# Performance work log

Hardware: AMD Instinct MI355X
Metric: run time of the kernel (lower is better)

The kernel has to match this reference:

```python
import jax, jax.numpy as jnp
import numpy as np

HEADS = 20


def cape_embed(f, P):
    # f: [b, s, d], P: [b, s, 4, 4]; rotate channel groups of 4 by P
    b, s, d = f.shape
    f4 = f.reshape(b, s, d // 4, 4)
    out = jnp.einsum('bsik,bskj->bsij', f4, P)
    return out.reshape(b, s, d)


def setup_inputs() -> dict:
    key = jax.random.key(0)
    ks = jax.random.split(key, 9)
    bt, l, d = 2, 1024, 1280  # (b*t_out, tokens, channels)
    t_out, b = 2, 1
    sd = 1.0 / np.sqrt(d)
    return {
        'hidden_states': jax.random.normal(ks[0], (bt, l, d), jnp.float32),
        'p_out': jax.random.normal(ks[1], (b, t_out, 4, 4), jnp.float32) * 0.5,
        'p_out_inv': jax.random.normal(ks[2], (b, t_out, 4, 4), jnp.float32) * 0.5,
        'Wq': jax.random.normal(ks[3], (d, d), jnp.float32) * sd,
        'Wk': jax.random.normal(ks[4], (d, d), jnp.float32) * sd,
        'Wv': jax.random.normal(ks[5], (d, d), jnp.float32) * sd,
        'Wo': jax.random.normal(ks[6], (d, d), jnp.float32) * sd,
        'bo': jnp.zeros((d,), jnp.float32),
    }


def reference(hidden_states, p_out, p_out_inv, Wq, Wk, Wv, Wo, bo):
    residual = hidden_states  # [(b t_out), l, d]
    b = p_out.shape[0]
    t_out = p_out.shape[1]
    bt, l, d = hidden_states.shape
    s = t_out * l
    hd = d // HEADS
    scale = hd ** -0.5

    # rearrange '(b t_out) l d -> b (t_out l) d'
    hs = hidden_states.reshape(b, s, d)

    q = hs @ Wq
    k = hs @ Wk
    v = hs @ Wv

    # repeat per-frame CAPE matrices over spatial tokens: 'b t f g -> b (t l) f g'
    Pq = jnp.repeat(p_out_inv, l, axis=1)  # [b, s, 4, 4]
    Pk = jnp.repeat(p_out, l, axis=1)      # self-attn: p_in := p_out
    q = cape_embed(q, Pq)
    k = cape_embed(k, Pk)

    # head split: [b, s, d] -> [b, h, s, hd]
    qh = q.reshape(b, s, HEADS, hd).transpose(0, 2, 1, 3)
    kh = k.reshape(b, s, HEADS, hd).transpose(0, 2, 1, 3)
    vh = v.reshape(b, s, HEADS, hd).transpose(0, 2, 1, 3)

    scores = jnp.einsum('bhsd,bhtd->bhst', qh, kh) * scale
    probs = jax.nn.softmax(scores, axis=-1)
    out = jnp.einsum('bhst,bhtd->bhsd', probs, vh)

    out = out.transpose(0, 2, 1, 3).reshape(b, s, d)
    out = out @ Wo + bo

    # rearrange 'b (t_out l) d -> (b t_out) l d'
    out = out.reshape(bt, l, d)
    out = out + residual  # residual_connection; rescale_output_factor = 1.0
    return out
```

## Files before the change

### kernel.cpp

```cpp
#include <hip/hip_runtime.h>

typedef short short8 __attribute__((ext_vector_type(8)));
typedef short short4v __attribute__((ext_vector_type(4)));
typedef float f32x4 __attribute__((ext_vector_type(4)));
typedef float float4v __attribute__((ext_vector_type(4)));
typedef __bf16 bf16x8 __attribute__((ext_vector_type(8)));
typedef _Float16 half4 __attribute__((ext_vector_type(4)));
typedef _Float16 half2v __attribute__((ext_vector_type(2)));

__device__ __forceinline__ short f2bf(float x) {
  unsigned u = __builtin_bit_cast(unsigned, x);
  u += 0x7fffu + ((u >> 16) & 1u);
  return (short)(u >> 16);
}

__device__ __forceinline__ f32x4 mfma16(short8 a, short8 b, f32x4 c) {
  return __builtin_amdgcn_mfma_f32_16x16x32_bf16(
      __builtin_bit_cast(bf16x8, a), __builtin_bit_cast(bf16x8, b), c, 0, 0, 0);
}

__device__ __forceinline__ void async16(void* lds, const void* g) {
  __builtin_amdgcn_global_load_lds(
      (const __attribute__((address_space(1))) unsigned*)g,
      (__attribute__((address_space(3))) unsigned*)lds, 16, 0, 0);
}

__global__ __launch_bounds__(256) void capeT_all_kernel(
    const float* __restrict__ Wq, const float* __restrict__ Wk,
    const float* __restrict__ Wv, const float* __restrict__ Wo,
    const float* __restrict__ p_inv, const float* __restrict__ p_out,
    float qscale, short* __restrict__ BT0, short* __restrict__ BT1,
    short* __restrict__ wo_t, const float* __restrict__ hs,
    short* __restrict__ hs_bf) {
  const int ND = 1280, KD = 1280;
  const size_t SEC = (size_t)1280 * 1280;
  int z = blockIdx.z;
  int tx = threadIdx.x, ty = threadIdx.y;
  if (z == 4) {
    int t = ty * 32 + tx;
    int base = ((blockIdx.y * 40 + blockIdx.x) * 256 + t) * 2;
    const int n4 = 2048 * 1280 / 4;
#pragma unroll
    for (int r = 0; r < 2; r++) {
      int i = base + r;
      if (i < n4) {
        float4v v = *(const float4v*)(hs + (size_t)i * 4);
        short4v o;
#pragma unroll
        for (int j = 0; j < 4; j++) o[j] = f2bf(v[j]);
        *(short4v*)(hs_bf + (size_t)i * 4) = o;
      }
    }
    return;
  }
  const float* W;
  const float* P;
  float scale = 1.0f;
  short *d0, *d1;
  if (z == 0) { W = Wq; P = p_inv; scale = qscale; d0 = BT0; d1 = BT1; }
  else if (z == 1) { W = Wk; P = p_out; d0 = BT0 + SEC; d1 = BT1 + SEC; }
  else if (z == 2) { W = Wv; P = nullptr; d0 = BT0 + 2 * SEC; d1 = BT1 + 2 * SEC; }
  else { W = Wo; P = nullptr; d0 = wo_t; d1 = nullptr; }

  __shared__ float tile[32][33];
  int bn = blockIdx.x * 32, bk = blockIdx.y * 32;
  for (int i = ty; i < 32; i += 8)
    tile[i][tx] = W[(size_t)(bk + i) * ND + bn + tx];
  __syncthreads();
  for (int c = ty; c < 32; c += 8) {
    float v0, v1;
    if (P) {
      int g = c & ~3, jj = c & 3;
      float a0 = 0.f, a1 = 0.f;
#pragma unroll
      for (int j = 0; j < 4; j++) {
        float wv = tile[tx][g + j];
        a0 += wv * P[j * 4 + jj];
        a1 += wv * P[16 + j * 4 + jj];
      }
      v0 = a0 * scale;
      v1 = a1 * scale;
    } else {
      v0 = v1 = tile[tx][c] * scale;
    }
    size_t o = (size_t)(bn + c) * KD + bk + tx;
    d0[o] = f2bf(v0);
    if (d1) d1[o] = f2bf(v1);
  }
}


__global__ __launch_bounds__(256) void gemm128_qkv_kernel(
    const short* __restrict__ A, const short* __restrict__ B0,
    const short* __restrict__ B1, int M, int N, int K,
    short* __restrict__ qb, short* __restrict__ ktl,
    _Float16* __restrict__ vtl) {
  __shared__ __align__(16) short As[2][128][32];
  __shared__ __align__(16) short Bs[2][128][32];
  int tid = threadIdx.x;
  int l = tid & 63, w = tid >> 6;
  int wr = w >> 1, wc = w & 1;
  int lr = l & 15, lg = l >> 4;
  int bm = blockIdx.y * 128, bn = blockIdx.x * 128;
  const short* BT = (bm >= 1024) ? B1 : B0;
  f32x4 acc[4][4] = {};

  auto stage = [&](int b, int k0) {
    const short* ga = A + (size_t)(bm + (tid >> 2)) * K + k0 + (tid & 3) * 8;
    const short* gb = BT + (size_t)(bn + (tid >> 2)) * K + k0 + (tid & 3) * 8;
    char* la = (char*)&As[b][0][0] + w * 1024;
    char* lb = (char*)&Bs[b][0][0] + w * 1024;
    async16(la, ga);
    async16(la + 4096, ga + (size_t)64 * K);
    async16(lb, gb);
    async16(lb + 4096, gb + (size_t)64 * K);
  };

  auto compute = [&](int b) {
    const short* Ab = &As[b][0][0];
    const short* Bb = &Bs[b][0][0];
    short8 af[4], bf_[4];
#pragma unroll
    for (int mi = 0; mi < 4; mi++)
      af[mi] = *(const short8*)(Ab + (wr * 64 + mi * 16 + lr) * 32 + lg * 8);
#pragma unroll
    for (int nj = 0; nj < 4; nj++)
      bf_[nj] = *(const short8*)(Bb + (wc * 64 + nj * 16 + lr) * 32 + lg * 8);
#pragma unroll
    for (int mi = 0; mi < 4; mi++)
#pragma unroll
      for (int nj = 0; nj < 4; nj++)
        acc[mi][nj] = mfma16(af[mi], bf_[nj], acc[mi][nj]);
  };

  int nk = K >> 5;
  stage(0, 0);
  for (int ks = 0; ks < nk; ks += 2) {
    __syncthreads();
    if (ks + 1 < nk) stage(1, (ks + 1) << 5);
    compute(0);
    __syncthreads();
    if (ks + 2 < nk) stage(0, (ks + 2) << 5);
    compute(1);
  }

#pragma unroll
  for (int mi = 0; mi < 4; mi++)
#pragma unroll
    for (int nj = 0; nj < 4; nj++)
#pragma unroll
      for (int i = 0; i < 4; i++) {
        int row = bm + wr * 64 + mi * 16 + lg * 4 + i;
        int col = bn + wc * 64 + nj * 16 + lr;
        float v = acc[mi][nj][i];
        int s = row;
        if (col < 1280) {
          qb[(((size_t)(col >> 6)) * 2048 + s) * 64 + (col & 63)] = f2bf(v);
        } else if (col < 2560) {
          int cc = col - 1280;
          int h = cc >> 6, d = cc & 63;
          int kt = s >> 6, r = s & 63;
          int kcol = (((d >> 3) ^ (r & 7)) << 3) | (d & 7);
          ktl[(((size_t)h * 32 + kt) * 64 + r) * 64 + kcol] = f2bf(v);
        } else {
          int cc = col - 2560;
          int h = cc >> 6, dv = cc & 63;
          int kt = s >> 6, key = s & 63;
          int sub = key >> 5, k5 = key & 31;
          int g = k5 >> 2;
          int vidx = sub * 2048 + g * 256 + ((dv ^ g) << 2) + (k5 & 3);
          vtl[((size_t)h * 32 + kt) * 4096 + vidx] = (_Float16)v;
        }
      }
}


__global__ __launch_bounds__(256) void gemm64_o_kernel(
    const short* __restrict__ A, const short* __restrict__ BT,
    int M, int N, int K, const float* __restrict__ bias,
    const float* __restrict__ resid, float* __restrict__ out) {
  __shared__ __align__(16) short As[2][64][32];
  __shared__ __align__(16) short Bs[2][64][32];
  int tid = threadIdx.x;
  int l = tid & 63, w = tid >> 6;
  int wr = w >> 1, wc = w & 1;
  int lr = l & 15, lg = l >> 4;
  int bm = blockIdx.y * 64, bn = blockIdx.x * 64;
  f32x4 acc[2][2] = {};

  auto stage = [&](int b, int k0) {
    const short* ga = A + (size_t)(bm + (tid >> 2)) * K + k0 + (tid & 3) * 8;
    const short* gb = BT + (size_t)(bn + (tid >> 2)) * K + k0 + (tid & 3) * 8;
    async16((char*)&As[b][0][0] + w * 1024, ga);
    async16((char*)&Bs[b][0][0] + w * 1024, gb);
  };

  auto compute = [&](int b) {
    const short* Ab = &As[b][0][0];
    const short* Bb = &Bs[b][0][0];
    short8 af[2], bf_[2];
#pragma unroll
    for (int mi = 0; mi < 2; mi++)
      af[mi] = *(const short8*)(Ab + (wr * 32 + mi * 16 + lr) * 32 + lg * 8);
#pragma unroll
    for (int nj = 0; nj < 2; nj++)
      bf_[nj] = *(const short8*)(Bb + (wc * 32 + nj * 16 + lr) * 32 + lg * 8);
#pragma unroll
    for (int mi = 0; mi < 2; mi++)
#pragma unroll
      for (int nj = 0; nj < 2; nj++)
        acc[mi][nj] = mfma16(af[mi], bf_[nj], acc[mi][nj]);
  };

  int nk = K >> 5;
  stage(0, 0);
  for (int ks = 0; ks < nk; ks += 2) {
    __syncthreads();
    if (ks + 1 < nk) stage(1, (ks + 1) << 5);
    compute(0);
    __syncthreads();
    if (ks + 2 < nk) stage(0, (ks + 2) << 5);
    compute(1);
  }

#pragma unroll
  for (int mi = 0; mi < 2; mi++)
#pragma unroll
    for (int nj = 0; nj < 2; nj++)
#pragma unroll
      for (int i = 0; i < 4; i++) {
        int row = bm + wr * 32 + mi * 16 + lg * 4 + i;
        int col = bn + wc * 32 + nj * 16 + lr;
        out[(size_t)row * N + col] =
            acc[mi][nj][i] + bias[col] + resid[(size_t)row * N + col];
      }
}

__global__ __launch_bounds__(256) void attn_kernel(
    const short* __restrict__ qb, const short* __restrict__ k_tiled,
    const _Float16* __restrict__ v_tiled, float* __restrict__ opart,
    float2* __restrict__ ml) {
  const int S = 2048, HD = 64;
  int h = blockIdx.x;
  int qblk = blockIdx.y;
  int half = blockIdx.z;
  int sbase = half * 32;
  int tid = threadIdx.x;
  int w = tid >> 6, l = tid & 63;
  int lr = l & 15, lg = l >> 4;
  int q0 = qblk * 64 + w * 16;

  __shared__ __align__(16) short Kl[2][32][64];
  __shared__ __align__(16) _Float16 Vl[2][2048];

  const short* qptr = qb + ((size_t)h * S + q0 + lr) * HD;
  short8 qf0 = *(const short8*)(qptr + lg * 8);
  short8 qf1 = *(const short8*)(qptr + 32 + lg * 8);

  auto stageKV = [&](int b, int ts) {
    int kt = ts >> 1, sub = ts & 1;
    const short* gk = k_tiled + ((size_t)h * 32 + kt) * 4096 + sub * 2048 + tid * 8;
    const _Float16* gv = v_tiled + ((size_t)h * 32 + kt) * 4096 + sub * 2048 + tid * 8;
    async16((char*)&Kl[b][0][0] + w * 1024, gk);
    async16((char*)&Vl[b][0] + w * 1024, gv);
  };

  float m = -1e30f, lsum = 0.f;
  f32x4 oacc[4] = {};

  auto compute_tile = [&](int buf) {
    const short* Kb = &Kl[buf][0][0];
    const _Float16* Vb = &Vl[buf][0];
    f32x4 st[2];
    __builtin_amdgcn_s_setprio(1);
#pragma unroll
    for (int kk = 0; kk < 2; kk++) {
      int r = kk * 16 + lr;
      int sw = r & 7;
      short8 kf0 = *(const short8*)(Kb + r * 64 + ((lg ^ sw) << 3));
      short8 kf1 = *(const short8*)(Kb + r * 64 + (((4 + lg) ^ sw) << 3));
      f32x4 s0 = {};
      s0 = mfma16(kf0, qf0, s0);
      s0 = mfma16(kf1, qf1, s0);
      st[kk] = s0;
    }
    __builtin_amdgcn_s_setprio(0);
    float m0 = fmaxf(fmaxf(st[0][0], st[0][1]), fmaxf(st[0][2], st[0][3]));
    float m1 = fmaxf(fmaxf(st[1][0], st[1][1]), fmaxf(st[1][2], st[1][3]));
    float pmax = fmaxf(m0, m1);
    if (!__all(pmax <= m + 8.0f)) {
      float tm = pmax;
      tm = fmaxf(tm, __shfl_xor(tm, 16));
      tm = fmaxf(tm, __shfl_xor(tm, 32));
      float mnew = fmaxf(m, tm);
      float fac = __builtin_amdgcn_exp2f(m - mnew);
      lsum *= fac;
#pragma unroll
      for (int i = 0; i < 4; i++) {
        float fi = __shfl(fac, lg * 4 + i);
#pragma unroll
        for (int nb = 0; nb < 4; nb++) oacc[nb][i] *= fi;
      }
      m = mnew;
    }
    half4 pf[2];
    float ps[2];
#pragma unroll
    for (int kk = 0; kk < 2; kk++) {
      float p0 = __builtin_amdgcn_exp2f(st[kk][0] - m);
      float p1 = __builtin_amdgcn_exp2f(st[kk][1] - m);
      float p2 = __builtin_amdgcn_exp2f(st[kk][2] - m);
      float p3 = __builtin_amdgcn_exp2f(st[kk][3] - m);
      half2v lo = __builtin_bit_cast(half2v, __builtin_amdgcn_cvt_pkrtz(p0, p1));
      half2v hi = __builtin_bit_cast(half2v, __builtin_amdgcn_cvt_pkrtz(p2, p3));
      pf[kk][0] = lo[0]; pf[kk][1] = lo[1];
      pf[kk][2] = hi[0]; pf[kk][3] = hi[1];
      ps[kk] = (p0 + p1) + (p2 + p3);
    }
    lsum += ps[0] + ps[1];
#pragma unroll
    for (int kk = 0; kk < 2; kk++) {
      half4 vf[4];
#pragma unroll
      for (int nb = 0; nb < 4; nb++) {
        int dv = nb * 16 + lr;
        int g = (kk << 2) + lg;
        vf[nb] = *(const half4*)(Vb + (g << 8) + ((dv ^ g) << 2));
      }
      __builtin_amdgcn_s_setprio(1);
#pragma unroll
      for (int nb = 0; nb < 4; nb++)
        oacc[nb] = __builtin_amdgcn_mfma_f32_16x16x16f16(pf[kk], vf[nb], oacc[nb], 0, 0, 0);
      __builtin_amdgcn_s_setprio(0);
    }
  };

  stageKV(0, sbase);
  for (int t2 = 0; t2 < 32; t2 += 2) {
    __syncthreads();
    if (t2 + 1 < 32) stageKV(1, sbase + t2 + 1);
    compute_tile(0);
    __syncthreads();
    if (t2 + 2 < 32) stageKV(0, sbase + t2 + 2);
    compute_tile(1);
  }

  lsum += __shfl_xor(lsum, 16);
  lsum += __shfl_xor(lsum, 32);

  size_t blk = (size_t)half * 640 + h * 32 + qblk;
  float* obase = opart + blk * 4096;
#pragma unroll
  for (int i = 0; i < 4; i++) {
    int ql = w * 16 + lg * 4 + i;
#pragma unroll
    for (int nb = 0; nb < 4; nb++)
      obase[ql * 64 + nb * 16 + lr] = oacc[nb][i];
  }
  if (lg == 0) {
    float2 v;
    v.x = m;
    v.y = lsum;
    ml[blk * 64 + w * 16 + lr] = v;
  }
}

__global__ __launch_bounds__(256) void attn_combine_kernel(
    const float* __restrict__ opart, const float2* __restrict__ ml,
    short* __restrict__ attn_out) {
  int h = blockIdx.x, qb = blockIdx.y;
  int t = threadIdx.x;
  int ql = t >> 2, dq = (t & 3) * 16;
  size_t blk = (size_t)h * 32 + qb;
  float2 ml0 = ml[blk * 64 + ql];
  float2 ml1 = ml[(size_t)640 * 64 + blk * 64 + ql];
  float M = fmaxf(ml0.x, ml1.x);
  float a0 = __builtin_amdgcn_exp2f(ml0.x - M);
  float a1 = __builtin_amdgcn_exp2f(ml1.x - M);
  float inv = 1.0f / (ml0.y * a0 + ml1.y * a1);
  float s0 = a0 * inv, s1 = a1 * inv;
  const float* o0 = opart + blk * 4096 + ql * 64 + dq;
  const float* o1 = o0 + (size_t)640 * 4096;
  int row = qb * 64 + ql;
  short* dst = attn_out + (size_t)row * 1280 + h * 64 + dq;
#pragma unroll
  for (int d = 0; d < 16; d += 4) {
    float4v v0 = *(const float4v*)(o0 + d);
    float4v v1 = *(const float4v*)(o1 + d);
    short4v o;
#pragma unroll
    for (int j = 0; j < 4; j++) o[j] = f2bf(v0[j] * s0 + v1[j] * s1);
    *(short4v*)(dst + d) = o;
  }
}


extern "C" void kernel_launch(void* const* d_in, const int* in_sizes, int n_in,
                              void* d_out, int out_size, void* d_ws, size_t ws_size,
                              hipStream_t stream) {
  const float* hs = (const float*)d_in[0];
  const float* p_out = (const float*)d_in[1];
  const float* p_inv = (const float*)d_in[2];
  const float* Wq = (const float*)d_in[3];
  const float* Wk = (const float*)d_in[4];
  const float* Wv = (const float*)d_in[5];
  const float* Wo = (const float*)d_in[6];
  const float* bo = (const float*)d_in[7];
  float* out = (float*)d_out;
  char* ws = (char*)d_ws;

  short* hs_bf = (short*)(ws + 0);
  short* BT0 = (short*)(ws + 5242880);
  short* BT1 = (short*)(ws + 15073280);
  short* wo_t = (short*)(ws + 24903680);
  short* q_bf = (short*)(ws + 28180480);
  short* k_tiled = (short*)(ws + 33423360);
  _Float16* v_tiled = (_Float16*)(ws + 38666240);
  short* attn_bf = (short*)(ws + 43909120);
  float* opart = (float*)(ws + 0);
  float2* ml = (float2*)(ws + 22020096);

  const float QSCALE = 0.125f * 1.44269504f;

  capeT_all_kernel<<<dim3(40, 40, 5), dim3(32, 8), 0, stream>>>(
      Wq, Wk, Wv, Wo, p_inv, p_out, QSCALE, BT0, BT1, wo_t, hs, hs_bf);

  gemm128_qkv_kernel<<<dim3(30, 16), 256, 0, stream>>>(
      hs_bf, BT0, BT1, 2048, 3840, 1280, q_bf, k_tiled, v_tiled);

  attn_kernel<<<dim3(20, 32, 2), 256, 0, stream>>>(
      q_bf, k_tiled, v_tiled, opart, ml);

  attn_combine_kernel<<<dim3(20, 32), 256, 0, stream>>>(opart, ml, attn_bf);

  gemm64_o_kernel<<<dim3(20, 32), 256, 0, stream>>>(
      attn_bf, wo_t, 2048, 1280, 1280, bo, hs, out);
}
```

Before: 122.4 us.

## Remap workgroup IDs for XCD locality and vectorize V-tile epilogue stores

Applies an XCD-aware workgroup remapping in the QKV GEMM, the output GEMM and the attention kernel. Consecutive remapped tiles, which share A/B rows or the same head's K/V, then land on the same chiplet and its L2. Also restructures the QKV epilogue so the four V values per lane are written as one packed half4 store instead of four scalar stores. The remapping assumes the grid size is divisible by 8 and hardcodes the attention grid dimensions (20x32x2). A mismatch would silently misassign tiles.

New measurement: 118.4 us. -3.2%, faster.

```diff
diff --git a/kernel.cpp b/kernel.cpp
--- a/kernel.cpp
+++ b/kernel.cpp
@@ -101,7 +101,11 @@
   int l = tid & 63, w = tid >> 6;
   int wr = w >> 1, wc = w & 1;
   int lr = l & 15, lg = l >> 4;
-  int bm = blockIdx.y * 128, bn = blockIdx.x * 128;
+  int nwg = gridDim.x * gridDim.y;
+  int orig = blockIdx.y * gridDim.x + blockIdx.x;
+  int wgid = (orig & 7) * (nwg >> 3) + (orig >> 3);
+  int bxs = wgid % gridDim.x, bys = wgid / gridDim.x;
+  int bm = bys * 128, bn = bxs * 128;
   const short* BT = (bm >= 1024) ? B1 : B0;
   f32x4 acc[4][4] = {};
 
@@ -147,31 +151,37 @@
 #pragma unroll
   for (int mi = 0; mi < 4; mi++)
 #pragma unroll
-    for (int nj = 0; nj < 4; nj++)
-#pragma unroll
-      for (int i = 0; i < 4; i++) {
-        int row = bm + wr * 64 + mi * 16 + lg * 4 + i;
-        int col = bn + wc * 64 + nj * 16 + lr;
-        float v = acc[mi][nj][i];
-        int s = row;
-        if (col < 1280) {
-          qb[(((size_t)(col >> 6)) * 2048 + s) * 64 + (col & 63)] = f2bf(v);
-        } else if (col < 2560) {
-          int cc = col - 1280;
-          int h = cc >> 6, d = cc & 63;
+    for (int nj = 0; nj < 4; nj++) {
+      int s0 = bm + wr * 64 + mi * 16 + lg * 4;
+      int col = bn + wc * 64 + nj * 16 + lr;
+      if (col < 1280) {
+#pragma unroll
+        for (int i = 0; i < 4; i++)
+          qb[(((size_t)(col >> 6)) * 2048 + s0 + i) * 64 + (col & 63)] =
+              f2bf(acc[mi][nj][i]);
+      } else if (col < 2560) {
+        int cc = col - 1280;
+        int h = cc >> 6, d = cc & 63;
+#pragma unroll
+        for (int i = 0; i < 4; i++) {
+          int s = s0 + i;
           int kt = s >> 6, r = s & 63;
           int kcol = (((d >> 3) ^ (r & 7)) << 3) | (d & 7);
-          ktl[(((size_t)h * 32 + kt) * 64 + r) * 64 + kcol] = f2bf(v);
-        } else {
-          int cc = col - 2560;
-          int h = cc >> 6, dv = cc & 63;
-          int kt = s >> 6, key = s & 63;
-          int sub = key >> 5, k5 = key & 31;
-          int g = k5 >> 2;
-          int vidx = sub * 2048 + g * 256 + ((dv ^ g) << 2) + (k5 & 3);
-          vtl[((size_t)h * 32 + kt) * 4096 + vidx] = (_Float16)v;
+          ktl[(((size_t)h * 32 + kt) * 64 + r) * 64 + kcol] = f2bf(acc[mi][nj][i]);
         }
-      }
+      } else {
+        int cc = col - 2560;
+        int h = cc >> 6, dv = cc & 63;
+        int kt = s0 >> 6, key0 = s0 & 63;
+        int sub = key0 >> 5, g = (key0 & 31) >> 2;
+        half4 o;
+#pragma unroll
+        for (int i = 0; i < 4; i++) o[i] = (_Float16)acc[mi][nj][i];
+        size_t vaddr = ((size_t)h * 32 + kt) * 4096 + sub * 2048 + g * 256 +
+                       ((dv ^ g) << 2);
+        *(half4*)(vtl + vaddr) = o;
+      }
+    }
 }
 
 
@@ -185,7 +195,11 @@
   int l = tid & 63, w = tid >> 6;
   int wr = w >> 1, wc = w & 1;
   int lr = l & 15, lg = l >> 4;
-  int bm = blockIdx.y * 64, bn = blockIdx.x * 64;
+  int nwg = gridDim.x * gridDim.y;
+  int orig = blockIdx.y * gridDim.x + blockIdx.x;
+  int wgid = (orig & 7) * (nwg >> 3) + (orig >> 3);
+  int bxs = wgid % gridDim.x, bys = wgid / gridDim.x;
+  int bm = bys * 64, bn = bxs * 64;
   f32x4 acc[2][2] = {};
 
   auto stage = [&](int b, int k0) {
@@ -241,9 +255,12 @@
     const _Float16* __restrict__ v_tiled, float* __restrict__ opart,
     float2* __restrict__ ml) {
   const int S = 2048, HD = 64;
-  int h = blockIdx.x;
-  int qblk = blockIdx.y;
-  int half = blockIdx.z;
+  int orig = (blockIdx.z * 32 + blockIdx.y) * 20 + blockIdx.x;
+  int wgid = (orig & 7) * 160 + (orig >> 3);
+  int h = wgid / 64;
+  int rem = wgid - h * 64;
+  int qblk = rem & 31;
+  int half = rem >> 5;
   int sbase = half * 32;
   int tid = threadIdx.x;
   int w = tid >> 6, l = tid & 63;
```
